# Kernel optimization log

Measured on AMD Instinct MI355X. Metric: run time of the kernel, lower is better.

The kernel has to match this reference:

```python
import jax, jax.numpy as jnp
import numpy as np

BS = 4
N_NODES = 10000
N_FEAT = 64
HID = 128
N_LAYERS = 4
HID_FC = 512
N_CLASSES = 10
N_EDGES = 160000


def setup_inputs() -> dict:
    key = jax.random.key(0)
    ks = jax.random.split(key, 10)
    x = jax.random.normal(ks[0], (BS, N_NODES, N_FEAT), jnp.float32)
    edge_index = jax.random.randint(ks[1], (2, N_EDGES), 0, N_NODES, dtype=jnp.int32)
    # batch[b*N_NODES + i] = b, matching x.view(num_nodes*bs, -1) row-major flatten
    batch = jnp.repeat(jnp.arange(BS, dtype=jnp.int32), N_NODES)
    W1 = jax.random.normal(ks[2], (N_FEAT, HID), jnp.float32) * (N_FEAT ** -0.5)
    b1 = jax.random.normal(ks[3], (HID,), jnp.float32) * 0.01
    Ws = jax.random.normal(ks[4], (N_LAYERS - 1, HID, HID), jnp.float32) * (HID ** -0.5)
    bconvs = jax.random.normal(ks[5], (N_LAYERS - 1, HID), jnp.float32) * 0.01
    lin1_w = jax.random.normal(ks[6], (N_LAYERS * HID, HID_FC), jnp.float32) * ((N_LAYERS * HID) ** -0.5)
    lin1_b = jax.random.normal(ks[7], (HID_FC,), jnp.float32) * 0.01
    lin2_w = jax.random.normal(ks[8], (HID_FC, N_CLASSES), jnp.float32) * (HID_FC ** -0.5)
    lin2_b = jax.random.normal(ks[9], (N_CLASSES,), jnp.float32) * 0.01
    return {"x": x, "edge_index": edge_index, "batch": batch,
            "W1": W1, "b1": b1, "Ws": Ws, "bconvs": bconvs,
            "lin1_w": lin1_w, "lin1_b": lin1_b, "lin2_w": lin2_w, "lin2_b": lin2_b}


def _gcn_norm(edge_index, n):
    # PyG GCNConv: add self-loops, symmetric normalization D^-1/2 (A+I) D^-1/2
    loops = jnp.arange(n, dtype=edge_index.dtype)
    src = jnp.concatenate([edge_index[0], loops])
    dst = jnp.concatenate([edge_index[1], loops])
    deg = jnp.zeros((n,), jnp.float32).at[dst].add(1.0)
    dinv = jnp.where(deg > 0, jax.lax.rsqrt(deg), 0.0)
    return src, dst, dinv[src] * dinv[dst]


def reference(x, edge_index, batch, W1, b1, Ws, bconvs, lin1_w, lin1_b, lin2_w, lin2_b):
    bs, n, _ = x.shape
    src, dst, norm = _gcn_norm(edge_index, n)

    def gcn(h, W, b):
        m = (h @ W)[:, src, :] * norm[None, :, None]          # [bs, E+n, H]
        agg = jax.vmap(lambda mm: jax.ops.segment_sum(mm, dst, num_segments=n))(m)
        return agg + b

    h = jax.nn.relu(gcn(x, W1, b1))
    xs = [h]
    for i in range(Ws.shape[0]):
        h = jax.nn.relu(gcn(h, Ws[i], bconvs[i]))
        xs.append(h)
    # torch.stack(xs, -1).view(bs, n, -1): per-channel layer interleave
    h = jnp.stack(xs, -1).reshape(bs, n, -1)                   # [bs, n, L*H]
    flat = h.reshape(bs * n, -1)
    summed = jax.ops.segment_sum(flat, batch, num_segments=bs)
    counts = jax.ops.segment_sum(jnp.ones((bs * n,), flat.dtype), batch, num_segments=bs)
    pooled = summed / counts[:, None]                          # global_mean_pool
    h = jax.nn.relu(pooled @ lin1_w + lin1_b)
    # dropout p=0.5 is inference-disabled (training=False)
    logits = h @ lin2_w + lin2_b
    return jax.nn.log_softmax(logits, axis=-1)
```

## Files before the change

### kernel.cpp

```cpp
#include <hip/hip_runtime.h>
#include <hip/hip_bf16.h>
#include <math.h>

#define N_NODES 10000
#define N_EDGES 160000
#define BS      4
#define N_TOT   (BS * N_NODES)
#define HID     128
#define NPC     10
#define CHUNKS  (N_NODES/NPC)
#define HID_FC  512
#define N_CLASSES 10
#define N_LAYERS  4
#define DEG_CAP 64
#define ZERO_INT4 325000

using bf16x8 = __attribute__((ext_vector_type(8))) short;
using f32x4  = __attribute__((ext_vector_type(4))) float;
using f32x2  = __attribute__((ext_vector_type(2))) float;

__device__ __forceinline__ unsigned bf_rne(float x) {
    unsigned b = __float_as_uint(x);
    return (b + 0x7fffu + ((b >> 16) & 1u)) >> 16;
}
__device__ __forceinline__ float bf2f(unsigned hi16) { return __uint_as_float(hi16 << 16); }

#if __has_builtin(__builtin_amdgcn_cvt_pk_f32_fp8) && __has_builtin(__builtin_amdgcn_cvt_pk_fp8_f32)
#define HW_FP8 1
#else
#define HW_FP8 0
#endif

__device__ __forceinline__ float fp8_dec1(unsigned b) {
    unsigned s = (b & 0x80u) << 24;
    unsigned em = b & 0x7Fu;
    float mag;
    if (em >= 8u) mag = __uint_as_float((((em >> 3) + 120u) << 23) | ((em & 7u) << 20));
    else          mag = (float)em * 0x1p-9f;
    return __uint_as_float(s | __float_as_uint(mag));
}

__device__ __forceinline__ unsigned fp8_enc(float x) {
#if HW_FP8
    return (unsigned)(__builtin_amdgcn_cvt_pk_fp8_f32(x, x, 0, false) & 0xFF);
#else
    unsigned s = (__float_as_uint(x) >> 24) & 0x80u;
    float ax = fabsf(x);
    unsigned r;
    if (ax >= 0x1p-6f) {
        if (ax > 448.f) r = 0x7Eu;
        else {
            unsigned b = __float_as_uint(ax);
            unsigned t = b + 0x7FFFFu + ((b >> 20) & 1u);
            r = (t >> 20) - 960u;
        }
    } else {
        r = (unsigned)__float2int_rn(ax * 512.f);
    }
    return s | r;
#endif
}

__device__ __forceinline__ float2 fp8x2_dec(unsigned u) {
#if HW_FP8
    f32x2 r = __builtin_amdgcn_cvt_pk_f32_fp8((int)(u & 0xFFFFu), false);
    return make_float2(r[0], r[1]);
#else
    return make_float2(fp8_dec1(u & 0xFFu), fp8_dec1((u >> 8) & 0xFFu));
#endif
}

__global__ __launch_bounds__(256) void k_prep(const float* __restrict__ x,
                                              const float* __restrict__ W1,
                                              const float* __restrict__ Ws,
                                              int4* __restrict__ zbase,
                                              ushort* __restrict__ x_bf,
                                              ushort* __restrict__ wt_hi,
                                              ushort* __restrict__ wt_lo) {
    const int gt = blockIdx.x * 256 + threadIdx.x, NT = gridDim.x * 256;
    for (int i = gt; i < ZERO_INT4; i += NT) zbase[i] = make_int4(0, 0, 0, 0);
    for (int i = gt; i < 640000; i += NT) {
        float4 v = ((const float4*)x)[i];
        ushort4 o;
        o.x = (ushort)bf_rne(v.x); o.y = (ushort)bf_rne(v.y);
        o.z = (ushort)bf_rne(v.z); o.w = (ushort)bf_rne(v.w);
        ((ushort4*)x_bf)[i] = o;
    }
    for (int i = gt; i < 57344; i += NT) {
        float v;
        if (i < 8192) { int c = i >> 6, k = i & 63; v = W1[k * HID + c]; }
        else {
            int tt = i - 8192, li = tt >> 14, rem = tt & 16383;
            int c = rem >> 7, k = rem & 127;
            v = Ws[li * 16384 + k * HID + c];
        }
        unsigned hi = bf_rne(v);
        unsigned lo = bf_rne(v - bf2f(hi));
        wt_hi[i] = (ushort)hi;
        wt_lo[i] = (ushort)lo;
    }
}

__global__ void k_count(const int* __restrict__ ei, int* __restrict__ counts) {
    int e = blockIdx.x * 256 + threadIdx.x;
    if (e < N_EDGES) atomicAdd(&counts[ei[N_EDGES + e]], 1);
}

__global__ void k_fill(const int* __restrict__ ei, const int* __restrict__ counts,
                       int* __restrict__ cursor, int2* __restrict__ csr) {
    int e = blockIdx.x * 256 + threadIdx.x;
    if (e < N_EDGES) {
        int s = ei[e], d = ei[N_EDGES + e];
        float ws = rsqrtf((float)(counts[s] + 1));
        int pos = atomicAdd(&cursor[d], 1);
        if (pos < DEG_CAP)
            csr[(d << 6) + pos] = make_int2(s, __float_as_int(ws));
    }
}

template<int K>
__global__ __launch_bounds__(256) void k_mm(const ushort* __restrict__ A,
                                            const ushort* __restrict__ Bt_hi,
                                            const ushort* __restrict__ Bt_lo,
                                            unsigned char* __restrict__ outF8) {
    constexpr int NS = K / 32;
    const int lane = threadIdx.x & 63;
    const int w    = threadIdx.x >> 6;
    const int row_base = blockIdx.x * 128 + w * 32;
    const int lr = lane & 15, lg = lane >> 4;

    bf16x8 a[2][NS];
    #pragma unroll
    for (int rh = 0; rh < 2; ++rh) {
        int r = row_base + rh * 16 + lr;
        if (r > N_TOT - 1) r = N_TOT - 1;
        const ushort* ap = A + (size_t)r * K + lg * 8;
        #pragma unroll
        for (int s = 0; s < NS; ++s)
            a[rh][s] = *(const bf16x8*)(ap + s * 32);
    }

    f32x4 acc[2][8];
    #pragma unroll
    for (int rh = 0; rh < 2; ++rh)
        #pragma unroll
        for (int n = 0; n < 8; ++n)
            acc[rh][n] = (f32x4){0.f, 0.f, 0.f, 0.f};

    #pragma unroll
    for (int n = 0; n < 8; ++n) {
        const ushort* bp = Bt_hi + (size_t)(n * 16 + lr) * K + lg * 8;
        const ushort* bq = Bt_lo + (size_t)(n * 16 + lr) * K + lg * 8;
        #pragma unroll
        for (int s = 0; s < NS; ++s) {
            bf16x8 bh = *(const bf16x8*)(bp + s * 32);
            bf16x8 bl = *(const bf16x8*)(bq + s * 32);
            acc[0][n] = __builtin_amdgcn_mfma_f32_16x16x32_bf16(a[0][s], bh, acc[0][n], 0, 0, 0);
            acc[1][n] = __builtin_amdgcn_mfma_f32_16x16x32_bf16(a[1][s], bh, acc[1][n], 0, 0, 0);
            acc[0][n] = __builtin_amdgcn_mfma_f32_16x16x32_bf16(a[0][s], bl, acc[0][n], 0, 0, 0);
            acc[1][n] = __builtin_amdgcn_mfma_f32_16x16x32_bf16(a[1][s], bl, acc[1][n], 0, 0, 0);
        }
    }

    #pragma unroll
    for (int rh = 0; rh < 2; ++rh) {
        int rb = row_base + rh * 16 + lg * 4;
        #pragma unroll
        for (int n = 0; n < 8; ++n) {
            int col = n * 16 + lr;
            #pragma unroll
            for (int j = 0; j < 4; ++j) {
                int r = rb + j;
                if (r < N_TOT)
                    outF8[(size_t)r * HID + col] = (unsigned char)fp8_enc(acc[rh][n][j]);
            }
        }
    }
}

__global__ __launch_bounds__(128) void k_agg(const ushort* __restrict__ tmp8,
                                             const int* __restrict__ counts,
                                             const int2* __restrict__ csr,
                                             const float* __restrict__ bias,
                                             unsigned* __restrict__ houtw,
                                             float* __restrict__ partial) {
    const int id = blockIdx.x;
    const int b = (id & 7) >> 1;
    const int chunk = ((id >> 3) << 1) | (id & 1);
    const int w = threadIdx.x >> 6, l = threadIdx.x & 63;
    const ushort* tb = tmp8 + (size_t)b * N_NODES * 64;
    const float2 bv = ((const float2*)bias)[l];
    float2 pool = {0.f, 0.f};
    const int n0 = chunk * NPC + w * (NPC / 2);
    for (int n = n0; n < n0 + NPC / 2; ++n) {
        int cnt = counts[n];
        const float dn = rsqrtf((float)(cnt + 1));
        if (cnt > DEG_CAP) cnt = DEG_CAP;
        const int no = (cnt + 7) >> 3;
        const float2 self = fp8x2_dec(tb[(size_t)n * 64 + l]);
        float ax[8], ay[8];
        ax[0] = dn * self.x; ay[0] = dn * self.y;
        #pragma unroll
        for (int i = 1; i < 8; ++i) { ax[i] = 0.f; ay[i] = 0.f; }
        const int4* cp = (const int4*)(csr + ((size_t)n << 6));
        for (int q = 0; q < no; ++q) {
            int4 q0 = cp[4 * q], q1 = cp[4 * q + 1], q2 = cp[4 * q + 2], q3 = cp[4 * q + 3];
            unsigned u0 = tb[(size_t)q0.x * 64 + l];
            unsigned u1 = tb[(size_t)q0.z * 64 + l];
            unsigned u2 = tb[(size_t)q1.x * 64 + l];
            unsigned u3 = tb[(size_t)q1.z * 64 + l];
            unsigned u4 = tb[(size_t)q2.x * 64 + l];
            unsigned u5 = tb[(size_t)q2.z * 64 + l];
            unsigned u6 = tb[(size_t)q3.x * 64 + l];
            unsigned u7 = tb[(size_t)q3.z * 64 + l];
            float w0 = __int_as_float(q0.y), w1 = __int_as_float(q0.w);
            float w2 = __int_as_float(q1.y), w3 = __int_as_float(q1.w);
            float w4 = __int_as_float(q2.y), w5 = __int_as_float(q2.w);
            float w6 = __int_as_float(q3.y), w7 = __int_as_float(q3.w);
            float2 f0 = fp8x2_dec(u0), f1 = fp8x2_dec(u1);
            float2 f2 = fp8x2_dec(u2), f3 = fp8x2_dec(u3);
            float2 f4 = fp8x2_dec(u4), f5 = fp8x2_dec(u5);
            float2 f6 = fp8x2_dec(u6), f7 = fp8x2_dec(u7);
            ax[0] = fmaf(w0, f0.x, ax[0]); ay[0] = fmaf(w0, f0.y, ay[0]);
            ax[1] = fmaf(w1, f1.x, ax[1]); ay[1] = fmaf(w1, f1.y, ay[1]);
            ax[2] = fmaf(w2, f2.x, ax[2]); ay[2] = fmaf(w2, f2.y, ay[2]);
            ax[3] = fmaf(w3, f3.x, ax[3]); ay[3] = fmaf(w3, f3.y, ay[3]);
            ax[4] = fmaf(w4, f4.x, ax[4]); ay[4] = fmaf(w4, f4.y, ay[4]);
            ax[5] = fmaf(w5, f5.x, ax[5]); ay[5] = fmaf(w5, f5.y, ay[5]);
            ax[6] = fmaf(w6, f6.x, ax[6]); ay[6] = fmaf(w6, f6.y, ay[6]);
            ax[7] = fmaf(w7, f7.x, ax[7]); ay[7] = fmaf(w7, f7.y, ay[7]);
        }
        float sx = ((ax[0] + ax[1]) + (ax[2] + ax[3])) + ((ax[4] + ax[5]) + (ax[6] + ax[7]));
        float sy = ((ay[0] + ay[1]) + (ay[2] + ay[3])) + ((ay[4] + ay[5]) + (ay[6] + ay[7]));
        float rx = fmaxf(fmaf(dn, sx, bv.x), 0.f);
        float ry = fmaxf(fmaf(dn, sy, bv.y), 0.f);
        houtw[((size_t)b * N_NODES + n) * 64 + l] = bf_rne(rx) | (bf_rne(ry) << 16);
        pool.x += rx; pool.y += ry;
    }
    __shared__ float2 pw[64];
    if (w == 1) pw[l] = pool;
    __syncthreads();
    if (w == 0) {
        pool.x += pw[l].x; pool.y += pw[l].y;
        ((float2*)partial)[((size_t)b * CHUNKS + chunk) * 64 + l] = pool;
    }
}

__global__ void k_reduce(const float* __restrict__ partial, float* __restrict__ pooled) {
    int l = blockIdx.x >> 2, b = blockIdx.x & 3, c = threadIdx.x;
    const float* p = partial + (size_t)(l * BS + b) * CHUNKS * HID + c;
    float s0 = 0, s1 = 0, s2 = 0, s3 = 0;
    for (int ch = 0; ch < CHUNKS; ch += 4) {
        s0 += p[(ch + 0) * HID];
        s1 += p[(ch + 1) * HID];
        s2 += p[(ch + 2) * HID];
        s3 += p[(ch + 3) * HID];
    }
    pooled[(size_t)(l * BS + b) * HID + c] = ((s0 + s1) + (s2 + s3)) * (1.0f / N_NODES);
}

__global__ __launch_bounds__(256) void k_lin1(const float* __restrict__ pooled,
                                              const float* __restrict__ w,
                                              const float* __restrict__ bias,
                                              float* __restrict__ h1) {
    __shared__ float pf[BS][HID_FC];
    __shared__ float red[8][32][BS];
    const int t = threadIdx.x;
    const int o0 = blockIdx.x * 32;
    for (int i = t; i < BS * HID_FC; i += 256) {
        int b = i >> 9, f = i & 511;
        int l = f & 3, cc = f >> 2;
        pf[b][f] = pooled[(size_t)(l * BS + b) * HID + cc];
    }
    __syncthreads();
    const int o = t & 31, kq = t >> 5;
    float acc[BS] = {0.f, 0.f, 0.f, 0.f};
    #pragma unroll 4
    for (int k = kq * 64; k < kq * 64 + 64; ++k) {
        float wv = w[(size_t)k * HID_FC + o0 + o];
        #pragma unroll
        for (int b = 0; b < BS; ++b) acc[b] = fmaf(pf[b][k], wv, acc[b]);
    }
    #pragma unroll
    for (int b = 0; b < BS; ++b) red[kq][o][b] = acc[b];
    __syncthreads();
    if (t < 128) {
        int oo = t & 31, b = t >> 5;
        float s = 0.f;
        #pragma unroll
        for (int q = 0; q < 8; ++q) s += red[q][oo][b];
        s += bias[o0 + oo];
        h1[(size_t)b * HID_FC + o0 + oo] = fmaxf(s, 0.f);
    }
}

__global__ __launch_bounds__(512) void k_lin2(const float* __restrict__ h1,
                                              const float* __restrict__ w,
                                              const float* __restrict__ bias,
                                              float* __restrict__ out) {
    const int k = threadIdx.x;
    const int lane = k & 63, wv_id = k >> 6;
    float wrow[N_CLASSES];
    #pragma unroll
    for (int c = 0; c < N_CLASSES; ++c) wrow[c] = w[k * N_CLASSES + c];
    float hv[BS];
    #pragma unroll
    for (int b = 0; b < BS; ++b) hv[b] = h1[b * HID_FC + k];
    float acc[BS][N_CLASSES];
    #pragma unroll
    for (int b = 0; b < BS; ++b)
        #pragma unroll
        for (int c = 0; c < N_CLASSES; ++c) acc[b][c] = hv[b] * wrow[c];
    #pragma unroll
    for (int off = 32; off >= 1; off >>= 1) {
        #pragma unroll
        for (int b = 0; b < BS; ++b)
            #pragma unroll
            for (int c = 0; c < N_CLASSES; ++c)
                acc[b][c] += __shfl_down(acc[b][c], off);
    }
    __shared__ float red[8][BS * N_CLASSES];
    if (lane == 0) {
        #pragma unroll
        for (int b = 0; b < BS; ++b)
            #pragma unroll
            for (int c = 0; c < N_CLASSES; ++c)
                red[wv_id][b * N_CLASSES + c] = acc[b][c];
    }
    __syncthreads();
    __shared__ float logits[BS][N_CLASSES];
    if (k < BS * N_CLASSES) {
        int b = k / N_CLASSES, c = k % N_CLASSES;
        float s = bias[c];
        #pragma unroll
        for (int q = 0; q < 8; ++q) s += red[q][k];
        logits[b][c] = s;
    }
    __syncthreads();
    if (k < BS) {
        float m = logits[k][0];
        for (int i = 1; i < N_CLASSES; ++i) m = fmaxf(m, logits[k][i]);
        float s = 0.f;
        for (int i = 0; i < N_CLASSES; ++i) s += expf(logits[k][i] - m);
        float lse = m + logf(s);
        for (int i = 0; i < N_CLASSES; ++i) out[k * N_CLASSES + i] = logits[k][i] - lse;
    }
}

extern "C" void kernel_launch(void* const* d_in, const int* in_sizes, int n_in,
                              void* d_out, int out_size, void* d_ws, size_t ws_size,
                              hipStream_t stream) {
    const float* x       = (const float*)d_in[0];
    const int*   ei      = (const int*)d_in[1];
    const float* W1      = (const float*)d_in[3];
    const float* b1      = (const float*)d_in[4];
    const float* Ws      = (const float*)d_in[5];
    const float* bconvs  = (const float*)d_in[6];
    const float* lin1_w  = (const float*)d_in[7];
    const float* lin1_b  = (const float*)d_in[8];
    const float* lin2_w  = (const float*)d_in[9];
    const float* lin2_b  = (const float*)d_in[10];
    float* out = (float*)d_out;

    char* base = (char*)d_ws;
    unsigned char* tmp8 = (unsigned char*)base; base += (size_t)N_TOT * HID;
    ushort* hA16   = (ushort*)base;    base += (size_t)N_TOT * HID * 2;
    ushort* x_bf   = (ushort*)base;    base += (size_t)N_TOT * 64 * 2;
    ushort* wt_hi  = (ushort*)base;    base += 57344 * 2;
    ushort* wt_lo  = (ushort*)base;    base += 57344 * 2;
    float*  partial= (float*)base;     base += (size_t)N_LAYERS * BS * CHUNKS * HID * 4;
    float*  pooled = (float*)base;     base += N_LAYERS * BS * HID * 4;
    float*  h1     = (float*)base;     base += BS * HID_FC * 4;
    int*    counts = (int*)base;       base += N_NODES * 4;
    int*    cursor = (int*)base;       base += N_NODES * 4;
    int2*   csr    = (int2*)base;

    const int GE = (N_EDGES + 255) / 256;

    k_prep<<<1024, 256, 0, stream>>>(x, W1, Ws, (int4*)counts, x_bf, wt_hi, wt_lo);
    k_count<<<GE, 256, 0, stream>>>(ei, counts);
    k_fill<<<GE, 256, 0, stream>>>(ei, counts, cursor, csr);

    const int agg_grid = BS * CHUNKS;
    const int mm_grid = (N_TOT + 127) / 128;

    k_mm<64><<<mm_grid, 256, 0, stream>>>(x_bf, wt_hi, wt_lo, tmp8);
    k_agg<<<agg_grid, 128, 0, stream>>>((const ushort*)tmp8, counts, csr, b1,
                                        (unsigned*)hA16, partial);
    for (int l = 1; l < N_LAYERS; ++l) {
        const ushort* whi = wt_hi + 8192 + (size_t)(l - 1) * 16384;
        const ushort* wlo = wt_lo + 8192 + (size_t)(l - 1) * 16384;
        const float* bl = bconvs + (size_t)(l - 1) * HID;
        k_mm<128><<<mm_grid, 256, 0, stream>>>(hA16, whi, wlo, tmp8);
        k_agg<<<agg_grid, 128, 0, stream>>>((const ushort*)tmp8, counts, csr, bl,
                                            (unsigned*)hA16,
                                            partial + (size_t)l * BS * CHUNKS * HID);
    }

    k_reduce<<<N_LAYERS * BS, HID, 0, stream>>>(partial, pooled);
    k_lin1<<<HID_FC / 32, 256, 0, stream>>>(pooled, lin1_w, lin1_b, h1);
    k_lin2<<<1, 512, 0, stream>>>(h1, lin2_w, lin2_b, out);
}
```

Baseline: 254.5 us.

## Interleave batch dimension in fp8 message buffer so one gather serves all batches

The matmul epilogue now writes the fp8 transformed features node-major, with all four batch elements for a node contiguous (512 bytes per node). The aggregation kernel then handles every batch for a chunk of nodes in one block, each lane loading 8 fp8 values with one 64-bit load and decoding them with packed converts. This lets one read of a CSR neighbor row feed all batches and makes each gather wider, aimed at cutting repeated CSR traffic and scattered small loads. Chunk size and the reduce kernel's thread layout change to suit, and the matmul store becomes more scattered.

```diff
diff --git a/kernel.cpp b/kernel.cpp
--- a/kernel.cpp
+++ b/kernel.cpp
@@ -7,7 +7,7 @@
 #define BS      4
 #define N_TOT   (BS * N_NODES)
 #define HID     128
-#define NPC     10
+#define NPC     4
 #define CHUNKS  (N_NODES/NPC)
 #define HID_FC  512
 #define N_CLASSES 10
@@ -61,12 +61,19 @@
 #endif
 }
 
-__device__ __forceinline__ float2 fp8x2_dec(unsigned u) {
+__device__ __forceinline__ void fp8x8_dec(uint2 u, float* f) {
 #if HW_FP8
-    f32x2 r = __builtin_amdgcn_cvt_pk_f32_fp8((int)(u & 0xFFFFu), false);
-    return make_float2(r[0], r[1]);
+    f32x2 p0 = __builtin_amdgcn_cvt_pk_f32_fp8((int)u.x, false);
+    f32x2 p1 = __builtin_amdgcn_cvt_pk_f32_fp8((int)u.x, true);
+    f32x2 p2 = __builtin_amdgcn_cvt_pk_f32_fp8((int)u.y, false);
+    f32x2 p3 = __builtin_amdgcn_cvt_pk_f32_fp8((int)u.y, true);
+    f[0] = p0[0]; f[1] = p0[1]; f[2] = p1[0]; f[3] = p1[1];
+    f[4] = p2[0]; f[5] = p2[1]; f[6] = p3[0]; f[7] = p3[1];
 #else
-    return make_float2(fp8_dec1(u & 0xFFu), fp8_dec1((u >> 8) & 0xFFu));
+    f[0] = fp8_dec1(u.x & 0xFFu);         f[1] = fp8_dec1((u.x >> 8) & 0xFFu);
+    f[2] = fp8_dec1((u.x >> 16) & 0xFFu); f[3] = fp8_dec1((u.x >> 24) & 0xFFu);
+    f[4] = fp8_dec1(u.y & 0xFFu);         f[5] = fp8_dec1((u.y >> 8) & 0xFFu);
+    f[6] = fp8_dec1((u.y >> 16) & 0xFFu); f[7] = fp8_dec1((u.y >> 24) & 0xFFu);
 #endif
 }
 
@@ -171,92 +178,136 @@
             #pragma unroll
             for (int j = 0; j < 4; ++j) {
                 int r = rb + j;
-                if (r < N_TOT)
-                    outF8[(size_t)r * HID + col] = (unsigned char)fp8_enc(acc[rh][n][j]);
+                if (r < N_TOT) {
+                    int b = r / N_NODES;
+                    int nd = r - b * N_NODES;
+                    outF8[(size_t)nd * 512 + b * 128 + col] =
+                        (unsigned char)fp8_enc(acc[rh][n][j]);
+                }
             }
         }
     }
 }
 
-__global__ __launch_bounds__(128) void k_agg(const ushort* __restrict__ tmp8,
+__global__ __launch_bounds__(128) void k_agg(const uint2* __restrict__ tmp8,
                                              const int* __restrict__ counts,
                                              const int2* __restrict__ csr,
                                              const float* __restrict__ bias,
-                                             unsigned* __restrict__ houtw,
+                                             uint4* __restrict__ hA,
                                              float* __restrict__ partial) {
-    const int id = blockIdx.x;
-    const int b = (id & 7) >> 1;
-    const int chunk = ((id >> 3) << 1) | (id & 1);
+    const int chunk = blockIdx.x;
     const int w = threadIdx.x >> 6, l = threadIdx.x & 63;
-    const ushort* tb = tmp8 + (size_t)b * N_NODES * 64;
-    const float2 bv = ((const float2*)bias)[l];
-    float2 pool = {0.f, 0.f};
+    const int b = l >> 4, c0 = (l & 15) * 8;
+    float bvv[8];
+    {
+        float4 b0 = *(const float4*)(bias + c0);
+        float4 b1 = *(const float4*)(bias + c0 + 4);
+        bvv[0] = b0.x; bvv[1] = b0.y; bvv[2] = b0.z; bvv[3] = b0.w;
+        bvv[4] = b1.x; bvv[5] = b1.y; bvv[6] = b1.z; bvv[7] = b1.w;
+    }
+    float pool[8];
+    #pragma unroll
+    for (int j = 0; j < 8; ++j) pool[j] = 0.f;
+
     const int n0 = chunk * NPC + w * (NPC / 2);
     for (int n = n0; n < n0 + NPC / 2; ++n) {
         int cnt = counts[n];
         const float dn = rsqrtf((float)(cnt + 1));
         if (cnt > DEG_CAP) cnt = DEG_CAP;
         const int no = (cnt + 7) >> 3;
-        const float2 self = fp8x2_dec(tb[(size_t)n * 64 + l]);
-        float ax[8], ay[8];
-        ax[0] = dn * self.x; ay[0] = dn * self.y;
-        #pragma unroll
-        for (int i = 1; i < 8; ++i) { ax[i] = 0.f; ay[i] = 0.f; }
+        float acc[8];
+        {
+            uint2 us = tmp8[n * 64 + l];
+            float sf[8];
+            fp8x8_dec(us, sf);
+            #pragma unroll
+            for (int j = 0; j < 8; ++j) acc[j] = dn * sf[j];
+        }
         const int4* cp = (const int4*)(csr + ((size_t)n << 6));
         for (int q = 0; q < no; ++q) {
             int4 q0 = cp[4 * q], q1 = cp[4 * q + 1], q2 = cp[4 * q + 2], q3 = cp[4 * q + 3];
-            unsigned u0 = tb[(size_t)q0.x * 64 + l];
-            unsigned u1 = tb[(size_t)q0.z * 64 + l];
-            unsigned u2 = tb[(size_t)q1.x * 64 + l];
-            unsigned u3 = tb[(size_t)q1.z * 64 + l];
-            unsigned u4 = tb[(size_t)q2.x * 64 + l];
-            unsigned u5 = tb[(size_t)q2.z * 64 + l];
-            unsigned u6 = tb[(size_t)q3.x * 64 + l];
-            unsigned u7 = tb[(size_t)q3.z * 64 + l];
+            uint2 u0 = tmp8[q0.x * 64 + l];
+            uint2 u1 = tmp8[q0.z * 64 + l];
+            uint2 u2 = tmp8[q1.x * 64 + l];
+            uint2 u3 = tmp8[q1.z * 64 + l];
+            uint2 u4 = tmp8[q2.x * 64 + l];
+            uint2 u5 = tmp8[q2.z * 64 + l];
+            uint2 u6 = tmp8[q3.x * 64 + l];
+            uint2 u7 = tmp8[q3.z * 64 + l];
             float w0 = __int_as_float(q0.y), w1 = __int_as_float(q0.w);
             float w2 = __int_as_float(q1.y), w3 = __int_as_float(q1.w);
             float w4 = __int_as_float(q2.y), w5 = __int_as_float(q2.w);
             float w6 = __int_as_float(q3.y), w7 = __int_as_float(q3.w);
-            float2 f0 = fp8x2_dec(u0), f1 = fp8x2_dec(u1);
-            float2 f2 = fp8x2_dec(u2), f3 = fp8x2_dec(u3);
-            float2 f4 = fp8x2_dec(u4), f5 = fp8x2_dec(u5);
-            float2 f6 = fp8x2_dec(u6), f7 = fp8x2_dec(u7);
-            ax[0] = fmaf(w0, f0.x, ax[0]); ay[0] = fmaf(w0, f0.y, ay[0]);
-            ax[1] = fmaf(w1, f1.x, ax[1]); ay[1] = fmaf(w1, f1.y, ay[1]);
-            ax[2] = fmaf(w2, f2.x, ax[2]); ay[2] = fmaf(w2, f2.y, ay[2]);
-            ax[3] = fmaf(w3, f3.x, ax[3]); ay[3] = fmaf(w3, f3.y, ay[3]);
-            ax[4] = fmaf(w4, f4.x, ax[4]); ay[4] = fmaf(w4, f4.y, ay[4]);
-            ax[5] = fmaf(w5, f5.x, ax[5]); ay[5] = fmaf(w5, f5.y, ay[5]);
-            ax[6] = fmaf(w6, f6.x, ax[6]); ay[6] = fmaf(w6, f6.y, ay[6]);
-            ax[7] = fmaf(w7, f7.x, ax[7]); ay[7] = fmaf(w7, f7.y, ay[7]);
-        }
-        float sx = ((ax[0] + ax[1]) + (ax[2] + ax[3])) + ((ax[4] + ax[5]) + (ax[6] + ax[7]));
-        float sy = ((ay[0] + ay[1]) + (ay[2] + ay[3])) + ((ay[4] + ay[5]) + (ay[6] + ay[7]));
-        float rx = fmaxf(fmaf(dn, sx, bv.x), 0.f);
-        float ry = fmaxf(fmaf(dn, sy, bv.y), 0.f);
-        houtw[((size_t)b * N_NODES + n) * 64 + l] = bf_rne(rx) | (bf_rne(ry) << 16);
-        pool.x += rx; pool.y += ry;
-    }
-    __shared__ float2 pw[64];
-    if (w == 1) pw[l] = pool;
+            float f[8];
+            fp8x8_dec(u0, f);
+            #pragma unroll
+            for (int j = 0; j < 8; ++j) acc[j] = fmaf(w0, f[j], acc[j]);
+            fp8x8_dec(u1, f);
+            #pragma unroll
+            for (int j = 0; j < 8; ++j) acc[j] = fmaf(w1, f[j], acc[j]);
+            fp8x8_dec(u2, f);
+            #pragma unroll
+            for (int j = 0; j < 8; ++j) acc[j] = fmaf(w2, f[j], acc[j]);
+            fp8x8_dec(u3, f);
+            #pragma unroll
+            for (int j = 0; j < 8; ++j) acc[j] = fmaf(w3, f[j], acc[j]);
+            fp8x8_dec(u4, f);
+            #pragma unroll
+            for (int j = 0; j < 8; ++j) acc[j] = fmaf(w4, f[j], acc[j]);
+            fp8x8_dec(u5, f);
+            #pragma unroll
+            for (int j = 0; j < 8; ++j) acc[j] = fmaf(w5, f[j], acc[j]);
+            fp8x8_dec(u6, f);
+            #pragma unroll
+            for (int j = 0; j < 8; ++j) acc[j] = fmaf(w6, f[j], acc[j]);
+            fp8x8_dec(u7, f);
+            #pragma unroll
+            for (int j = 0; j < 8; ++j) acc[j] = fmaf(w7, f[j], acc[j]);
+        }
+        float r[8];
+        #pragma unroll
+        for (int j = 0; j < 8; ++j) {
+            r[j] = fmaxf(fmaf(dn, acc[j], bvv[j]), 0.f);
+            pool[j] += r[j];
+        }
+        uint4 ov;
+        ov.x = bf_rne(r[0]) | (bf_rne(r[1]) << 16);
+        ov.y = bf_rne(r[2]) | (bf_rne(r[3]) << 16);
+        ov.z = bf_rne(r[4]) | (bf_rne(r[5]) << 16);
+        ov.w = bf_rne(r[6]) | (bf_rne(r[7]) << 16);
+        hA[(size_t)(b * N_NODES + n) * 16 + (c0 >> 3)] = ov;
+    }
+
+    __shared__ float pw[64][8];
+    if (w == 1) {
+        #pragma unroll
+        for (int j = 0; j < 8; ++j) pw[l][j] = pool[j];
+    }
     __syncthreads();
     if (w == 0) {
-        pool.x += pw[l].x; pool.y += pw[l].y;
-        ((float2*)partial)[((size_t)b * CHUNKS + chunk) * 64 + l] = pool;
-    }
-}
-
-__global__ void k_reduce(const float* __restrict__ partial, float* __restrict__ pooled) {
-    int l = blockIdx.x >> 2, b = blockIdx.x & 3, c = threadIdx.x;
-    const float* p = partial + (size_t)(l * BS + b) * CHUNKS * HID + c;
-    float s0 = 0, s1 = 0, s2 = 0, s3 = 0;
-    for (int ch = 0; ch < CHUNKS; ch += 4) {
-        s0 += p[(ch + 0) * HID];
-        s1 += p[(ch + 1) * HID];
-        s2 += p[(ch + 2) * HID];
-        s3 += p[(ch + 3) * HID];
-    }
-    pooled[(size_t)(l * BS + b) * HID + c] = ((s0 + s1) + (s2 + s3)) * (1.0f / N_NODES);
+        #pragma unroll
+        for (int j = 0; j < 8; ++j) pool[j] += pw[l][j];
+        float* pp = partial + ((size_t)b * CHUNKS + chunk) * HID + c0;
+        *(float4*)pp = make_float4(pool[0], pool[1], pool[2], pool[3]);
+        *(float4*)(pp + 4) = make_float4(pool[4], pool[5], pool[6], pool[7]);
+    }
+}
+
+__global__ __launch_bounds__(512) void k_reduce(const float* __restrict__ partial,
+                                                float* __restrict__ pooled) {
+    const int lb = blockIdx.x;
+    const int c = threadIdx.x & 127, qh = threadIdx.x >> 7;
+    const float* p = partial + (size_t)lb * CHUNKS * HID + c;
+    float s = 0.f;
+    const int e0 = qh * (CHUNKS / 4), e1 = e0 + CHUNKS / 4;
+    #pragma unroll 8
+    for (int ch = e0; ch < e1; ++ch) s += p[(size_t)ch * HID];
+    __shared__ float sm[4][128];
+    sm[qh][c] = s;
+    __syncthreads();
+    if (qh == 0)
+        pooled[(size_t)lb * HID + c] =
+            (sm[0][c] + sm[1][c] + sm[2][c] + sm[3][c]) * (1.0f / N_NODES);
 }
 
 __global__ __launch_bounds__(256) void k_lin1(const float* __restrict__ pooled,
@@ -363,7 +414,7 @@
     float* out = (float*)d_out;
 
     char* base = (char*)d_ws;
-    unsigned char* tmp8 = (unsigned char*)base; base += (size_t)N_TOT * HID;
+    unsigned char* tmp8 = (unsigned char*)base; base += (size_t)N_NODES * 512;
     ushort* hA16   = (ushort*)base;    base += (size_t)N_TOT * HID * 2;
     ushort* x_bf   = (ushort*)base;    base += (size_t)N_TOT * 64 * 2;
     ushort* wt_hi  = (ushort*)base;    base += 57344 * 2;
@@ -381,23 +432,23 @@
     k_count<<<GE, 256, 0, stream>>>(ei, counts);
     k_fill<<<GE, 256, 0, stream>>>(ei, counts, cursor, csr);
 
-    const int agg_grid = BS * CHUNKS;
+    const int agg_grid = CHUNKS;
     const int mm_grid = (N_TOT + 127) / 128;
 
     k_mm<64><<<mm_grid, 256, 0, stream>>>(x_bf, wt_hi, wt_lo, tmp8);
-    k_agg<<<agg_grid, 128, 0, stream>>>((const ushort*)tmp8, counts, csr, b1,
-                                        (unsigned*)hA16, partial);
+    k_agg<<<agg_grid, 128, 0, stream>>>((const uint2*)tmp8, counts, csr, b1,
+                                        (uint4*)hA16, partial);
     for (int l = 1; l < N_LAYERS; ++l) {
         const ushort* whi = wt_hi + 8192 + (size_t)(l - 1) * 16384;
         const ushort* wlo = wt_lo + 8192 + (size_t)(l - 1) * 16384;
         const float* bl = bconvs + (size_t)(l - 1) * HID;
         k_mm<128><<<mm_grid, 256, 0, stream>>>(hA16, whi, wlo, tmp8);
-        k_agg<<<agg_grid, 128, 0, stream>>>((const ushort*)tmp8, counts, csr, bl,
-                                            (unsigned*)hA16,
+        k_agg<<<agg_grid, 128, 0, stream>>>((const uint2*)tmp8, counts, csr, bl,
+                                            (uint4*)hA16,
                                             partial + (size_t)l * BS * CHUNKS * HID);
     }
 
-    k_reduce<<<N_LAYERS * BS, HID, 0, stream>>>(partial, pooled);
+    k_reduce<<<N_LAYERS * BS, 512, 0, stream>>>(partial, pooled);
     k_lin1<<<HID_FC / 32, 256, 0, stream>>>(pooled, lin1_w, lin1_b, h1);
     k_lin2<<<1, 512, 0, stream>>>(h1, lin2_w, lin2_b, out);
 }
```

Measured after the change: 263.0 us. +3.4%, slower.
